# Kernel tuning notes

Hardware: AMD Instinct MI355X
Metric: run time of the kernel (lower is better)

The kernel has to match this reference:

```python
import jax, jax.numpy as jnp
import numpy as np

H = 512

def _lstm_scan(xs, h0, c0, Wih, Whh, bih, bhh):
    # xs: [T,B,I]; PyTorch gate order i,f,g,o
    def step(carry, x):
        h, c = carry
        gates = x @ Wih.T + bih + h @ Whh.T + bhh  # [B,4H]
        i, f, g, o = jnp.split(gates, 4, axis=-1)
        c = jax.nn.sigmoid(f) * c + jax.nn.sigmoid(i) * jnp.tanh(g)
        h = jax.nn.sigmoid(o) * jnp.tanh(c)
        return (h, c), h
    (h, c), ys = jax.lax.scan(step, (h0, c0), xs)
    return ys, h, c


def setup_inputs() -> dict:
    key = jax.random.key(0)
    ks = jax.random.split(key, 12)
    T, B, I, O = 513, 128, 1, 1
    s = 1.0 / np.sqrt(H)
    u = lambda k, shp: jax.random.uniform(k, shp, jnp.float32, -s, s)
    return {
        "input_seq": jax.random.normal(ks[0], (T, B, I), jnp.float32),
        "h0": jnp.zeros((B, H), jnp.float32),
        "c0": jnp.zeros((B, H), jnp.float32),
        "lstm_Wih": u(ks[1], (4 * H, I)),
        "lstm_Whh": u(ks[2], (4 * H, H)),
        "lstm_bih": u(ks[3], (4 * H,)),
        "lstm_bhh": u(ks[4], (4 * H,)),
        "rnn_Wih": u(ks[5], (H, O)),
        "rnn_Whh": u(ks[6], (H, H)),
        "rnn_bih": u(ks[7], (H,)),
        "rnn_bhh": u(ks[8], (H,)),
        "lin_W": u(ks[9], (O, H)),
        "lin_b": u(ks[10], (O,)),
        "batch_size": 128,
        "pred_length": 32,
    }


def reference(input_seq, h0, c0, lstm_Wih, lstm_Whh, lstm_bih, lstm_bhh,
              rnn_Wih, rnn_Whh, rnn_bih, rnn_bhh, lin_W, lin_b,
              batch_size, pred_length):
    # Encoder LSTM over input_seq[:-1]
    enc_ys, h_enc, _ = _lstm_scan(input_seq[:-1], h0, c0,
                                  lstm_Wih, lstm_Whh, lstm_bih, lstm_bhh)
    enc_bth = jnp.transpose(enc_ys, (1, 0, 2))  # [B,T,H]

    def dec_step(carry, _):
        x, h = carry  # x: [B,1] last prediction, h: [B,H] RNN hidden
        h = jnp.tanh(x @ rnn_Wih.T + rnn_bih + h @ rnn_Whh.T + rnn_bhh)
        # Luong dot-product attention over encoder outputs
        scores = jnp.einsum('bth,bh->bt', enc_bth, h)
        w = jax.nn.softmax(scores, axis=-1)
        ctx = jnp.einsum('bt,bth->bh', w, enc_bth)
        out = jax.nn.relu(ctx @ lin_W.T + lin_b)  # [B,1]
        return (out, h), out

    x0 = input_seq[-1]  # [B,1]
    _, preds = jax.lax.scan(dec_step, (x0, h_enc), None, length=pred_length)
    return preds  # [pred_length, B, 1]
```

## Files before the change

kernel.cpp:

```cpp
#include <hip/hip_runtime.h>
#include <hip/hip_bf16.h>

typedef unsigned short u16;
typedef unsigned int u32;

#define HD 512
#define BATCH 128
#define TENC 512
#define WPAD 520

typedef float f32x4 __attribute__((ext_vector_type(4)));
typedef short s16x8 __attribute__((ext_vector_type(8)));

__device__ __forceinline__ u16 f2b(float f) {
    u32 u = __float_as_uint(f);
    u32 r = (u + 0x7FFFu + ((u >> 16) & 1u)) >> 16;
    return (u16)r;
}
__device__ __forceinline__ float b2f(u16 h) {
    return __uint_as_float(((u32)h) << 16);
}
__device__ __forceinline__ float sigm(float z) { return 1.0f / (1.0f + __expf(-z)); }
__device__ __forceinline__ float tanh_f(float z) { return 1.0f - 2.0f / (__expf(2.0f * z) + 1.0f); }

__global__ void init_misc(const float* __restrict__ h0, const float* __restrict__ rWhh,
                          u16* __restrict__ hbuf, u16* __restrict__ rT,
                          u32* __restrict__ flags) {
    int idx = blockIdx.x * 256 + threadIdx.x;
    if (idx < 2048) flags[idx] = 0u;
    if (idx < 65536) {
        int bg = idx >> 9, j = idx & 511;
        int g = bg >> 4, bl = bg & 15;
        hbuf[(size_t)(g * 2) * 8192 + bl * 512 + j] = f2b(h0[idx]);
    }
    for (int i = idx; i < 262144; i += 131072) {
        int k = i >> 9, j = i & 511;
        rT[i] = f2b(rWhh[j * 512 + k]);
    }
}

__global__ __launch_bounds__(512, 2) void enc_lstm(
    const float* __restrict__ xseq, const float* __restrict__ c0,
    const float* __restrict__ Wih, const float* __restrict__ Whh,
    const float* __restrict__ bih, const float* __restrict__ bhh,
    u16* __restrict__ enc, u32* __restrict__ hb32, u32* __restrict__ flags) {

    __shared__ u16 hlds[16 * WPAD];
    __shared__ float exg[16 * 132];
    __shared__ float bias_l[128];
    __shared__ float wih_l[128];

    const int tid = threadIdx.x;
    const int g = blockIdx.x & 7;
    const int sl = blockIdx.x >> 3;

    if (tid < 128) {
        int n = (tid >> 5) * 512 + sl * 32 + (tid & 31);
        bias_l[tid] = bih[n] + bhh[n];
        wih_l[tid] = Wih[n];
    }

    const int bT = tid >> 5, jl = tid & 31;
    float c = c0[(g * 16 + bT) * HD + sl * 32 + jl];

    const int lane = tid & 63, wv = tid >> 6;
    const int q = lane >> 4, cl = lane & 15;
    const int R = (wv >> 1) * 32 + (wv & 1) * 16;

    s16x8 bw[16];
    {
        int r = R + cl;
        int grow = (r >> 5) * 512 + sl * 32 + (r & 31);
        const float* wrow = Whh + (size_t)grow * 512;
        #pragma unroll
        for (int ks = 0; ks < 16; ++ks) {
            s16x8 v;
            #pragma unroll
            for (int j = 0; j < 8; ++j)
                v[j] = (short)f2b(wrow[ks * 32 + q * 8 + j]);
            bw[ks] = v;
        }
    }

    u32* flg = flags + g * 256;
    u32* hlds32 = (u32*)hlds;
    __syncthreads();

    for (int t = 0; t < TENC; ++t) {
        const u32* src32 = hb32 + (size_t)(g * 2 + (t & 1)) * 4096;
        #pragma unroll
        for (int i = 0; i < 8; ++i) {
            int idx = tid + i * 512;
            u32 v = __hip_atomic_load(src32 + idx, __ATOMIC_RELAXED,
                                      __HIP_MEMORY_SCOPE_AGENT);
            int b = idx >> 8, w = idx & 255;
            hlds32[b * 260 + w] = v;
        }
        float xv = xseq[t * BATCH + g * 16 + bT];
        __syncthreads();

        f32x4 acc = {0.f, 0.f, 0.f, 0.f};
        #pragma unroll
        for (int ks = 0; ks < 16; ++ks) {
            s16x8 av = *(const s16x8*)&hlds[cl * WPAD + ks * 32 + q * 8];
            acc = __builtin_amdgcn_mfma_f32_16x16x32_bf16(av, bw[ks], acc, 0, 0, 0);
        }
        #pragma unroll
        for (int r4 = 0; r4 < 4; ++r4)
            exg[(q * 4 + r4) * 132 + R + cl] = acc[r4];
        __syncthreads();

        const float* exb = &exg[bT * 132];
        float gi = exb[jl]      + xv * wih_l[jl]      + bias_l[jl];
        float gf = exb[32 + jl] + xv * wih_l[32 + jl] + bias_l[32 + jl];
        float gg = exb[64 + jl] + xv * wih_l[64 + jl] + bias_l[64 + jl];
        float go = exb[96 + jl] + xv * wih_l[96 + jl] + bias_l[96 + jl];
        c = sigm(gf) * c + sigm(gi) * tanh_f(gg);
        float hv = sigm(go) * tanh_f(c);
        u16 h16 = f2b(hv);
        int jgl = sl * 32 + jl;

        u32 me = (u32)h16;
        u32 up = (u32)__shfl_down((int)me, 1, 64);
        if ((jl & 1) == 0) {
            u32 pair = me | (up << 16);
            __hip_atomic_store(hb32 + (size_t)(g * 2 + ((t + 1) & 1)) * 4096
                                    + bT * 256 + (jgl >> 1),
                               pair, __ATOMIC_RELAXED, __HIP_MEMORY_SCOPE_AGENT);
        }

        __builtin_amdgcn_s_waitcnt(0);
        __syncthreads();
        if (tid == 0)
            __hip_atomic_store(&flg[sl * 16], (u32)(t + 1),
                               __ATOMIC_RELAXED, __HIP_MEMORY_SCOPE_AGENT);
        enc[((size_t)t * BATCH + g * 16 + bT) * HD + jgl] = h16;
        if (tid < 16) {
            while (__hip_atomic_load(&flg[tid * 16], __ATOMIC_RELAXED,
                                     __HIP_MEMORY_SCOPE_AGENT) < (u32)(t + 1))
                __builtin_amdgcn_s_sleep(1);
        }
        __atomic_signal_fence(__ATOMIC_SEQ_CST);
        __syncthreads();
    }
}

__global__ __launch_bounds__(512, 2) void dec_all(
    const float* __restrict__ xlast, const u16* __restrict__ enc,
    const u16* __restrict__ rT, const float* __restrict__ rWih,
    const float* __restrict__ rbih, const float* __restrict__ rbhh,
    const float* __restrict__ linW, const float* __restrict__ linb,
    float* __restrict__ dout) {

    __shared__ float hp[512];
    __shared__ float ctxl[8 * 512];
    __shared__ float red[512];
    __shared__ float mw[8], lw[8];
    __shared__ float xsh;

    const int tid = threadIdx.x;
    const int b = blockIdx.x;
    const int wv = tid >> 6, lane = tid & 63;

    hp[tid] = b2f(enc[(size_t)511 * BATCH * HD + b * HD + tid]);
    float x = xlast[b];
    const float bia = rbih[tid] + rbhh[tid];
    const float wih = rWih[tid];
    const float lwt = linW[tid];
    const float lb = linb[0];
    const uint4* rT4 = (const uint4*)rT;
    const u16* ebase = enc + (size_t)b * HD + lane * 8;
    __syncthreads();

    for (int s = 0; s < 32; ++s) {
        uint4 buf[4];
        #pragma unroll
        for (int i = 0; i < 4; ++i)
            buf[i] = *(const uint4*)(ebase + (size_t)(i * 8 + wv) * 65536);

        float pa[8] = {0, 0, 0, 0, 0, 0, 0, 0};
        const uint4* base = rT4 + (size_t)(wv * 64) * 64 + lane;
        #pragma unroll 4
        for (int kk = 0; kk < 64; ++kk) {
            float hk = hp[wv * 64 + kk];
            uint4 w = base[kk * 64];
            pa[0] = fmaf(hk, b2f((u16)(w.x & 0xFFFF)), pa[0]);
            pa[1] = fmaf(hk, b2f((u16)(w.x >> 16)),    pa[1]);
            pa[2] = fmaf(hk, b2f((u16)(w.y & 0xFFFF)), pa[2]);
            pa[3] = fmaf(hk, b2f((u16)(w.y >> 16)),    pa[3]);
            pa[4] = fmaf(hk, b2f((u16)(w.z & 0xFFFF)), pa[4]);
            pa[5] = fmaf(hk, b2f((u16)(w.z >> 16)),    pa[5]);
            pa[6] = fmaf(hk, b2f((u16)(w.w & 0xFFFF)), pa[6]);
            pa[7] = fmaf(hk, b2f((u16)(w.w >> 16)),    pa[7]);
        }
        #pragma unroll
        for (int i = 0; i < 8; ++i) ctxl[wv * 512 + lane * 8 + i] = pa[i];
        __syncthreads();

        float a = bia + x * wih;
        #pragma unroll
        for (int i = 0; i < 8; ++i) a += ctxl[i * 512 + tid];
        float hv = tanh_f(a);
        red[tid] = hv;
        __syncthreads();

        float h8[8];
        #pragma unroll
        for (int i = 0; i < 8; ++i) h8[i] = red[lane * 8 + i];
        float m = -1e30f, l = 0.f;
        float acc[8] = {0, 0, 0, 0, 0, 0, 0, 0};
        for (int blk = 0; blk < 16; ++blk) {
            uint4 nxt[4];
            if (blk < 15) {
                #pragma unroll
                for (int i = 0; i < 4; ++i)
                    nxt[i] = *(const uint4*)(ebase +
                               (size_t)((blk + 1) * 32 + i * 8 + wv) * 65536);
            }
            #pragma unroll
            for (int i = 0; i < 4; ++i) {
                uint4 ev = buf[i];
                float e[8];
                e[0] = b2f((u16)(ev.x & 0xFFFF)); e[1] = b2f((u16)(ev.x >> 16));
                e[2] = b2f((u16)(ev.y & 0xFFFF)); e[3] = b2f((u16)(ev.y >> 16));
                e[4] = b2f((u16)(ev.z & 0xFFFF)); e[5] = b2f((u16)(ev.z >> 16));
                e[6] = b2f((u16)(ev.w & 0xFFFF)); e[7] = b2f((u16)(ev.w >> 16));
                float sp = 0.f;
                #pragma unroll
                for (int j = 0; j < 8; ++j) sp = fmaf(e[j], h8[j], sp);
                #pragma unroll
                for (int mk = 1; mk < 64; mk <<= 1) sp += __shfl_xor(sp, mk, 64);
                if (sp > m) {
                    float sc = __expf(m - sp);
                    l *= sc;
                    #pragma unroll
                    for (int j = 0; j < 8; ++j) acc[j] *= sc;
                    m = sp;
                }
                float p = __expf(sp - m);
                l += p;
                #pragma unroll
                for (int j = 0; j < 8; ++j) acc[j] = fmaf(p, e[j], acc[j]);
            }
            #pragma unroll
            for (int i = 0; i < 4; ++i) buf[i] = nxt[i];
        }
        if (lane == 0) { mw[wv] = m; lw[wv] = l; }
        #pragma unroll
        for (int i = 0; i < 8; ++i) ctxl[wv * HD + lane * 8 + i] = acc[i];
        __syncthreads();

        float M = mw[0];
        #pragma unroll
        for (int i = 1; i < 8; ++i) M = fmaxf(M, mw[i]);
        float L = 0.f, aw[8];
        #pragma unroll
        for (int i = 0; i < 8; ++i) { aw[i] = __expf(mw[i] - M); L += aw[i] * lw[i]; }
        float cj = 0.f;
        #pragma unroll
        for (int i = 0; i < 8; ++i) cj = fmaf(aw[i], ctxl[i * HD + tid], cj);
        float r = cj * lwt;
        #pragma unroll
        for (int mk = 1; mk < 64; mk <<= 1) r += __shfl_xor(r, mk, 64);
        if (lane == 0) red[wv] = r;
        __syncthreads();
        if (tid == 0) {
            float o = (red[0] + red[1] + red[2] + red[3] +
                       red[4] + red[5] + red[6] + red[7]) / L + lb;
            o = fmaxf(o, 0.f);
            dout[s * BATCH + b] = o;
            xsh = o;
        }
        __syncthreads();
        x = xsh;
        hp[tid] = hv;
        __syncthreads();
    }
}

extern "C" void kernel_launch(void* const* d_in, const int* in_sizes, int n_in,
                              void* d_out, int out_size, void* d_ws, size_t ws_size,
                              hipStream_t stream) {
    const float* xseq = (const float*)d_in[0];
    const float* h0   = (const float*)d_in[1];
    const float* c0   = (const float*)d_in[2];
    const float* Wih  = (const float*)d_in[3];
    const float* Whh  = (const float*)d_in[4];
    const float* bih  = (const float*)d_in[5];
    const float* bhh  = (const float*)d_in[6];
    const float* rWih = (const float*)d_in[7];
    const float* rWhh = (const float*)d_in[8];
    const float* rbih = (const float*)d_in[9];
    const float* rbhh = (const float*)d_in[10];
    const float* linW = (const float*)d_in[11];
    const float* linb = (const float*)d_in[12];
    float* dout = (float*)d_out;

    char* ws = (char*)d_ws;
    u16* enc   = (u16*)ws;
    u16* rT    = (u16*)(ws + 67108864);
    u16* hbuf  = (u16*)(ws + 67108864 + 524288);
    u32* flags = (u32*)(ws + 67108864 + 524288 + 262144);

    init_misc<<<512, 256, 0, stream>>>(h0, rWhh, hbuf, rT, flags);
    enc_lstm<<<128, 512, 0, stream>>>(xseq, c0, Wih, Whh, bih, bhh, enc,
                                      (u32*)hbuf, flags);
    dec_all<<<128, 512, 0, stream>>>(xseq + 512 * BATCH, enc, rT, rWih,
                                     rbih, rbhh, linW, linb, dout);
}
```

Measured before the change: 2.779 ms.

## Replace per-step flag barrier with step-tagged 64-bit hidden-state words

The encoder LSTM used to publish each block's hidden-state slice, wait for stores to drain, then run a flag-based cross-block barrier with spinning and two extra __syncthreads per timestep. Now each published value is a 64-bit word that carries the packed bf16 pair plus the step number. Consumers spin directly on the data words until every tag matches the expected step, so the separate flag array and global barrier are gone. This removes a round trip and the block-wide synchronization from the serial 512-step critical path. In exchange it doubles the bytes read per hidden-state load and makes each thread poll its own words.

Measured after the change: 2.567 ms. 1.08x faster.

```diff
diff --git a/kernel.cpp b/kernel.cpp
--- a/kernel.cpp
+++ b/kernel.cpp
@@ -3,6 +3,7 @@
 
 typedef unsigned short u16;
 typedef unsigned int u32;
+typedef unsigned long long u64;
 
 #define HD 512
 #define BATCH 128
@@ -24,14 +25,21 @@
 __device__ __forceinline__ float tanh_f(float z) { return 1.0f - 2.0f / (__expf(2.0f * z) + 1.0f); }
 
 __global__ void init_misc(const float* __restrict__ h0, const float* __restrict__ rWhh,
-                          u16* __restrict__ hbuf, u16* __restrict__ rT,
-                          u32* __restrict__ flags) {
+                          u64* __restrict__ hb64, u16* __restrict__ rT) {
     int idx = blockIdx.x * 256 + threadIdx.x;
-    if (idx < 2048) flags[idx] = 0u;
     if (idx < 65536) {
-        int bg = idx >> 9, j = idx & 511;
-        int g = bg >> 4, bl = bg & 15;
-        hbuf[(size_t)(g * 2) * 8192 + bl * 512 + j] = f2b(h0[idx]);
+        int g   = idx >> 13;
+        int r   = idx & 8191;
+        int p   = r >> 12;
+        int ofs = r & 4095;
+        int b   = ofs >> 8, jp = ofs & 255;
+        u64 v = 0ull;
+        if (p == 0) {
+            const float* hrow = h0 + (size_t)(g * 16 + b) * HD + jp * 2;
+            u32 lo = (u32)f2b(hrow[0]) | ((u32)f2b(hrow[1]) << 16);
+            v = (u64)lo;
+        }
+        hb64[(size_t)(g * 2 + p) * 4096 + b * 256 + jp] = v;
     }
     for (int i = idx; i < 262144; i += 131072) {
         int k = i >> 9, j = i & 511;
@@ -43,7 +51,7 @@
     const float* __restrict__ xseq, const float* __restrict__ c0,
     const float* __restrict__ Wih, const float* __restrict__ Whh,
     const float* __restrict__ bih, const float* __restrict__ bhh,
-    u16* __restrict__ enc, u32* __restrict__ hb32, u32* __restrict__ flags) {
+    u16* __restrict__ enc, u64* __restrict__ hb64) {
 
     __shared__ u16 hlds[16 * WPAD];
     __shared__ float exg[16 * 132];
@@ -82,21 +90,36 @@
         }
     }
 
-    u32* flg = flags + g * 256;
     u32* hlds32 = (u32*)hlds;
     __syncthreads();
 
     for (int t = 0; t < TENC; ++t) {
-        const u32* src32 = hb32 + (size_t)(g * 2 + (t & 1)) * 4096;
+        const u64* src = hb64 + (size_t)(g * 2 + (t & 1)) * 4096;
+        const u32 want = (u32)t;
+        u64 vv[8];
+        #pragma unroll
+        for (int i = 0; i < 8; ++i)
+            vv[i] = __hip_atomic_load(src + tid + i * 512, __ATOMIC_RELAXED,
+                                      __HIP_MEMORY_SCOPE_AGENT);
+        float xv = xseq[t * BATCH + g * 16 + bT];
+        for (;;) {
+            bool ok = true;
+            #pragma unroll
+            for (int i = 0; i < 8; ++i) {
+                if ((u32)(vv[i] >> 32) != want) {
+                    ok = false;
+                    vv[i] = __hip_atomic_load(src + tid + i * 512, __ATOMIC_RELAXED,
+                                              __HIP_MEMORY_SCOPE_AGENT);
+                }
+            }
+            if (ok) break;
+        }
         #pragma unroll
         for (int i = 0; i < 8; ++i) {
             int idx = tid + i * 512;
-            u32 v = __hip_atomic_load(src32 + idx, __ATOMIC_RELAXED,
-                                      __HIP_MEMORY_SCOPE_AGENT);
             int b = idx >> 8, w = idx & 255;
-            hlds32[b * 260 + w] = v;
-        }
-        float xv = xseq[t * BATCH + g * 16 + bT];
+            hlds32[b * 260 + w] = (u32)vv[i];
+        }
         __syncthreads();
 
         f32x4 acc = {0.f, 0.f, 0.f, 0.f};
@@ -123,25 +146,12 @@
         u32 me = (u32)h16;
         u32 up = (u32)__shfl_down((int)me, 1, 64);
         if ((jl & 1) == 0) {
-            u32 pair = me | (up << 16);
-            __hip_atomic_store(hb32 + (size_t)(g * 2 + ((t + 1) & 1)) * 4096
+            u64 word = (u64)(me | (up << 16)) | ((u64)(u32)(t + 1) << 32);
+            __hip_atomic_store(hb64 + (size_t)(g * 2 + ((t + 1) & 1)) * 4096
                                     + bT * 256 + (jgl >> 1),
-                               pair, __ATOMIC_RELAXED, __HIP_MEMORY_SCOPE_AGENT);
-        }
-
-        __builtin_amdgcn_s_waitcnt(0);
-        __syncthreads();
-        if (tid == 0)
-            __hip_atomic_store(&flg[sl * 16], (u32)(t + 1),
-                               __ATOMIC_RELAXED, __HIP_MEMORY_SCOPE_AGENT);
+                               word, __ATOMIC_RELAXED, __HIP_MEMORY_SCOPE_AGENT);
+        }
         enc[((size_t)t * BATCH + g * 16 + bT) * HD + jgl] = h16;
-        if (tid < 16) {
-            while (__hip_atomic_load(&flg[tid * 16], __ATOMIC_RELAXED,
-                                     __HIP_MEMORY_SCOPE_AGENT) < (u32)(t + 1))
-                __builtin_amdgcn_s_sleep(1);
-        }
-        __atomic_signal_fence(__ATOMIC_SEQ_CST);
-        __syncthreads();
     }
 }
 
@@ -297,14 +307,12 @@
     float* dout = (float*)d_out;
 
     char* ws = (char*)d_ws;
-    u16* enc   = (u16*)ws;
-    u16* rT    = (u16*)(ws + 67108864);
-    u16* hbuf  = (u16*)(ws + 67108864 + 524288);
-    u32* flags = (u32*)(ws + 67108864 + 524288 + 262144);
-
-    init_misc<<<512, 256, 0, stream>>>(h0, rWhh, hbuf, rT, flags);
-    enc_lstm<<<128, 512, 0, stream>>>(xseq, c0, Wih, Whh, bih, bhh, enc,
-                                      (u32*)hbuf, flags);
+    u16* enc  = (u16*)ws;
+    u16* rT   = (u16*)(ws + 67108864);
+    u64* hb64 = (u64*)(ws + 67108864 + 524288);
+
+    init_misc<<<512, 256, 0, stream>>>(h0, rWhh, hb64, rT);
+    enc_lstm<<<128, 512, 0, stream>>>(xseq, c0, Wih, Whh, bih, bhh, enc, hb64);
     dec_all<<<128, 512, 0, stream>>>(xseq + 512 * BATCH, enc, rT, rWih,
                                      rbih, rbhh, linW, linb, dout);
 }
```
